# Kernel optimization log

Measured on AMD Instinct MI355X. Metric: run time of the kernel, lower is better.

## Reference

```python
import jax, jax.numpy as jnp
import numpy as np

P, A = 8, 65536            # poses, atoms per pose
N = P * A                  # total atoms
N1 = N + 1                 # kin nodes (node 0 = virtual root)


def _local_hts(dofs):
    """Per-node local homogeneous transform from bond DOFs.
    dofs[:,0]=phi (torsion), dofs[:,1]=theta (bond angle), dofs[:,2]=d (length).
    M = Rz(phi) @ Ry(theta) @ Trans_x(d)   (NeRF-style internal coordinates)."""
    phi, theta, d = dofs[:, 0], dofs[:, 1], dofs[:, 2]
    cp, sp = jnp.cos(phi), jnp.sin(phi)
    ct, st = jnp.cos(theta), jnp.sin(theta)
    z = jnp.zeros_like(phi)
    o = jnp.ones_like(phi)
    # R = Rz(phi) @ Ry(theta)
    r00, r01, r02 = cp * ct, -sp, cp * st
    r10, r11, r12 = sp * ct, cp, sp * st
    r20, r21, r22 = -st, z, ct
    # t = R @ [d,0,0]
    t0, t1, t2 = d * r00, d * r10, d * r20
    M = jnp.stack([
        jnp.stack([r00, r01, r02, t0], -1),
        jnp.stack([r10, r11, r12, t1], -1),
        jnp.stack([r20, r21, r22, t2], -1),
        jnp.stack([z, z, z, o], -1),
    ], -2)  # [N1,4,4]
    return M


def setup_inputs() -> dict:
    rng = np.random.default_rng(0)
    # tree: each node's parent is 1..4 nodes back (topologically sorted), root self-parented
    parents = np.zeros(N1, np.int32)
    idx = np.arange(1, N1)
    parents[1:] = np.maximum(idx - 1 - rng.integers(0, 4, size=N), 0).astype(np.int32)
    # kinforest.id: permutation mapping kin node (1..N) -> flat atom index
    kin_id = rng.permutation(N).astype(np.int32)
    # base DOFs (detached full_dofs): realistic bond geometry
    base = np.zeros((N1, 4), np.float32)
    base[:, 1] = rng.uniform(1.5, 2.2, N1)          # theta
    base[:, 2] = rng.normal(1.53, 0.02, N1)         # bond length
    masked = rng.uniform(-np.pi, np.pi, N1).astype(np.float32)  # torsion params
    bond_w = rng.uniform(0.5, 1.5, (P, A - 1)).astype(np.float32)
    pose_coords = np.zeros((P, A, 3), np.float32)
    return {
        "masked_dofs": jnp.asarray(masked),
        "base_dofs": jnp.asarray(base),
        "pose_coords": jnp.asarray(pose_coords),
        "bond_w": jnp.asarray(bond_w),
        "parents": jnp.asarray(parents),
        "kin_id": jnp.asarray(kin_id),
    }


def reference(masked_dofs, base_dofs, pose_coords, bond_w, parents, kin_id):
    # 1) write optimizable DOFs into full DOF tensor (dof_mask = torsion column)
    dofs = base_dofs.at[:, 0].set(masked_dofs)
    # 2) per-node local transforms; root = identity
    M = _local_hts(dofs)
    M = M.at[0].set(jnp.eye(4, dtype=M.dtype))
    # 3) forwardKin: compose parent->child transforms via pointer doubling
    n_iters = int(np.ceil(np.log2(N1)))
    def body(carry, _):
        G, p = carry
        G = jnp.einsum('nij,njk->nik', G[p], G)
        return (G, p[p]), None
    (G, _), _ = jax.lax.scan(body, (M, parents), None, length=n_iters)
    kincoords = G[1:, :3, 3]  # [N,3] global positions (skip root)
    # 4) scatter kin coords back into pose-stack coordinates
    flat = pose_coords.reshape(-1, 3).at[kin_id].set(kincoords)
    coords = flat.reshape(pose_coords.shape)  # [P,A,3]
    # 5) whole-pose scoring: weighted bonded quadratic energy per pose
    d = coords[:, 1:] - coords[:, :-1]
    energy = jnp.sum(bond_w * jnp.sum(d * d, -1), axis=-1)  # [P]
    return energy
```

## Files before the change

### kernel.cpp

```cpp
#include <hip/hip_runtime.h>

#define NN1    524289
#define PP     8
#define AA     65536
#define SEGLEN 64
#define NSEG   8193
#define CHUNK  33
#define NCHK   249
#define NE     (NCHK*4)

#define OFF_COORDS 0
#define OFF_NT   2097152
#define OFF_L1G  4194308
#define OFF_L1E  4587572
#define OFF_PREG 4620344
#define OFF_PREE 5013608
#define OFF_BCG  5046380
#define OFF_CLG  5058332
#define OFF_CLE  5070284

static __device__ __forceinline__ void set_ident(float* a){
  a[0]=1.f;a[1]=0.f;a[2]=0.f;a[3]=0.f;
  a[4]=0.f;a[5]=1.f;a[6]=0.f;a[7]=0.f;
  a[8]=0.f;a[9]=0.f;a[10]=1.f;a[11]=0.f;
}

static __device__ __forceinline__ void compose(const float* Aa, const float* B, float* O){
  #pragma unroll
  for(int r=0;r<3;r++){
    float a0=Aa[r*4+0],a1=Aa[r*4+1],a2=Aa[r*4+2],a3=Aa[r*4+3];
    O[r*4+0]=a0*B[0]+a1*B[4]+a2*B[8];
    O[r*4+1]=a0*B[1]+a1*B[5]+a2*B[9];
    O[r*4+2]=a0*B[2]+a1*B[6]+a2*B[10];
    O[r*4+3]=a0*B[3]+a1*B[7]+a2*B[11]+a3;
  }
}

static __device__ __forceinline__ void load12(const float4* b4, int idx, float* a){
  float4 x=b4[idx*3+0], y=b4[idx*3+1], z=b4[idx*3+2];
  a[0]=x.x;a[1]=x.y;a[2]=x.z;a[3]=x.w;
  a[4]=y.x;a[5]=y.y;a[6]=y.z;a[7]=y.w;
  a[8]=z.x;a[9]=z.y;a[10]=z.z;a[11]=z.w;
}
static __device__ __forceinline__ void store12(float4* b4, int idx, const float* a){
  b4[idx*3+0]=make_float4(a[0],a[1],a[2],a[3]);
  b4[idx*3+1]=make_float4(a[4],a[5],a[6],a[7]);
  b4[idx*3+2]=make_float4(a[8],a[9],a[10],a[11]);
}

static __device__ __forceinline__ void wave_scan(
    int w, int lane,
    const float* __restrict__ masked, const float4* __restrict__ base4,
    const int* __restrict__ parents,
    float G[12], int& pk)
{
  int i0 = w*SEGLEN;
  int i = i0 + lane;
  if(i == 0 || i >= NN1){
    set_ident(G); pk = 0xFF;
  } else {
    float4 b = base4[i];
    float phi = masked[i];
    float sp,cp,st,ct;
    __sincosf(phi,&sp,&cp);
    __sincosf(b.y,&st,&ct);
    float dd = b.z;
    G[0]=cp*ct; G[1]=-sp; G[2]=cp*st; G[3]=dd*G[0];
    G[4]=sp*ct; G[5]=cp;  G[6]=sp*st; G[7]=dd*G[4];
    G[8]=-st;   G[9]=0.f; G[10]=ct;   G[11]=dd*G[8];
    int rel = parents[i] - i0;
    pk = (rel >= 0) ? rel : (((rel+4)<<8) | 0xFF);
  }
  #pragma unroll
  for(int step=0; step<6; ++step){
    int ptr = pk & 0xFF;
    bool act = (ptr != 0xFF);
    int src = act ? ptr : lane;
    float g2[12];
    #pragma unroll
    for(int q=0;q<12;q++) g2[q] = __shfl(G[q], src, 64);
    int pk2 = __shfl(pk, src, 64);
    float ng[12];
    compose(g2, G, ng);
    #pragma unroll
    for(int q=0;q<12;q++) G[q] = act ? ng[q] : G[q];
    pk = act ? pk2 : pk;
  }
}

#define BSTEP(BX, EX) {                                                   \
    int s_ = s0 + q;                                                      \
    store12(PREG, s_*4+j, acc); PREE[s_*4+j] = ae;                        \
    float lg_[12];                                                        \
    _Pragma("unroll") for(int z=0;z<12;z++) lg_[z]=BX[z];                 \
    int le_ = EX;                                                         \
    if(q+3 < ns){ load12(L1G,(s_+3)*4+j, BX); EX = L1E[(s_+3)*4+j]; }     \
    int srcLane_ = laneBase + le_;                                        \
    float src_[12];                                                       \
    _Pragma("unroll") for(int z=0;z<12;z++) src_[z] = __shfl(acc[z], srcLane_, 64); \
    int se_ = __shfl(ae, srcLane_, 64);                                   \
    float nw_[12]; compose(src_, lg_, nw_);                               \
    _Pragma("unroll") for(int z=0;z<12;z++) acc[z]=nw_[z];                \
    ae = se_;                                                             \
    q++;                                                                  \
  }

static __device__ __forceinline__ void chunk_scan(
    int idx, int lane,
    const float4* __restrict__ L1G, const int* __restrict__ L1E,
    float4* __restrict__ PREG, int* __restrict__ PREE,
    float acc[12], int& ae)
{
  int g = idx>>2, j = idx&3;
  int laneBase = lane & ~3;
  int s0 = g*CHUNK;
  int ns = min(CHUNK, NSEG - s0);
  set_ident(acc); ae = j;
  float b0[12],b1[12],b2[12]; int e0=0,e1=0,e2=0;
  load12(L1G, s0*4+j, b0); e0 = L1E[s0*4+j];
  if(ns>1){ load12(L1G,(s0+1)*4+j,b1); e1 = L1E[(s0+1)*4+j]; }
  if(ns>2){ load12(L1G,(s0+2)*4+j,b2); e2 = L1E[(s0+2)*4+j]; }
  int q = 0;
  while(true){
    BSTEP(b0, e0); if(q>=ns) break;
    BSTEP(b1, e1); if(q>=ns) break;
    BSTEP(b2, e2); if(q>=ns) break;
  }
}

__global__ __launch_bounds__(1024) void fk1(
    const float* __restrict__ masked, const float4* __restrict__ base4,
    const int* __restrict__ parents,
    float4* __restrict__ L1G, int* __restrict__ L1E,
    float4* __restrict__ NT, float* __restrict__ out)
{
  if(blockIdx.x==0 && threadIdx.x < PP) out[threadIdx.x] = 0.f;
  int w = blockIdx.x*16 + (threadIdx.x>>6);
  if(w >= NSEG) return;
  int lane = threadIdx.x & 63;
  float G[12]; int pk;
  wave_scan(w, lane, masked, base4, parents, G, pk);
  int i = w*SEGLEN + lane;
  int tag = (pk>>8)&3;
  if(i < NN1){
    NT[i] = make_float4(G[3], G[7], G[11], __int_as_float(tag));
  }
  if(lane >= 60){
    int j = lane - 60;
    store12(L1G, w*4+j, G);
    L1E[w*4+j] = tag;
  }
}

__global__ __launch_bounds__(64) void fk2(
    const float4* __restrict__ L1G, const int* __restrict__ L1E,
    float4* __restrict__ PREG, int* __restrict__ PREE,
    float4* __restrict__ CLG, int* __restrict__ CLE)
{
  int idx = blockIdx.x*64 + threadIdx.x;
  if(idx >= NE) return;
  float acc[12]; int ae;
  chunk_scan(idx, threadIdx.x & 63, L1G, L1E, PREG, PREE, acc, ae);
  store12(CLG, idx, acc);
  CLE[idx] = ae;
}

__global__ __launch_bounds__(1024) void fk3(
    const float4* __restrict__ CLG, const int* __restrict__ CLE,
    float4* __restrict__ BCG)
{
  __shared__ float Lg[NE*12];
  __shared__ int   Le[NE];
  float4* Lg4 = (float4*)Lg;
  int tid = threadIdx.x;
  if(tid < NE){
    float a[12]; load12(CLG, tid, a);
    Lg4[tid*3+0]=make_float4(a[0],a[1],a[2],a[3]);
    Lg4[tid*3+1]=make_float4(a[4],a[5],a[6],a[7]);
    Lg4[tid*3+2]=make_float4(a[8],a[9],a[10],a[11]);
    Le[tid]=CLE[tid];
  }
  __syncthreads();
  for(int d=1; d<NCHK; d<<=1){
    float ng[12]; int ne2=0;
    bool doit = (tid<NE) && ((tid>>2)>=d);
    if(doit){
      int myE = Le[tid];
      int pe = ((tid>>2)-d)*4 + myE;
      float own[12], pg[12];
      load12(Lg4, tid, own);
      load12(Lg4, pe, pg);
      compose(pg, own, ng);
      ne2 = Le[pe];
    }
    __syncthreads();
    if(doit){
      Lg4[tid*3+0]=make_float4(ng[0],ng[1],ng[2],ng[3]);
      Lg4[tid*3+1]=make_float4(ng[4],ng[5],ng[6],ng[7]);
      Lg4[tid*3+2]=make_float4(ng[8],ng[9],ng[10],ng[11]);
      Le[tid]=ne2;
    }
    __syncthreads();
  }
  if(tid < NE){
    float b[12];
    if((tid>>2)==0){ set_ident(b); }
    else { load12(Lg4, tid-4, b); }
    store12(BCG, tid, b);
  }
}

__global__ __launch_bounds__(1024) void fk4(
    const int* __restrict__ kin, const float4* __restrict__ NT,
    const float4* __restrict__ PREG, const int* __restrict__ PREE,
    const float4* __restrict__ BCG,
    float4* __restrict__ coords)
{
  int w = blockIdx.x*16 + (threadIdx.x>>6);
  if(w >= NSEG) return;
  int lane = threadIdx.x & 63;
  int i = w*SEGLEN + lane;
  if(i == 0 || i >= NN1) return;
  float4 nt = NT[i];
  int tag = __float_as_int(nt.w) & 3;
  int c = w / CHUNK;
  int e = PREE[w*4+tag];
  float bg[12], pg[12], A[12];
  load12(BCG, c*4+e, bg);
  load12(PREG, w*4+tag, pg);
  compose(bg, pg, A);
  float x = A[0]*nt.x + A[1]*nt.y + A[2]*nt.z  + A[3];
  float y = A[4]*nt.x + A[5]*nt.y + A[6]*nt.z  + A[7];
  float z = A[8]*nt.x + A[9]*nt.y + A[10]*nt.z + A[11];
  coords[kin[i-1]] = make_float4(x, y, z, 0.f);
}

__global__ void fk5(const float4* __restrict__ coords, const float* __restrict__ bw,
                    float* __restrict__ out)
{
  int p = blockIdx.x >> 5;
  int sub = blockIdx.x & 31;
  int a0 = sub * 2048;
  int aend = min(a0 + 2048, AA - 1);
  float sum = 0.f;
  for(int a = a0 + (int)threadIdx.x; a < aend; a += 256){
    int r = p*AA + a;
    float4 c0 = coords[r], c1 = coords[r+1];
    float dx = c1.x-c0.x, dy = c1.y-c0.y, dz = c1.z-c0.z;
    sum += bw[p*(AA-1)+a]*(dx*dx+dy*dy+dz*dz);
  }
  #pragma unroll
  for(int off=32;off>0;off>>=1) sum += __shfl_down(sum, off, 64);
  __shared__ float red[4];
  int lane = threadIdx.x & 63, wid = threadIdx.x >> 6;
  if(lane==0) red[wid]=sum;
  __syncthreads();
  if(threadIdx.x==0){
    float tot = red[0]+red[1]+red[2]+red[3];
    atomicAdd(&out[p], tot);
  }
}

extern "C" void kernel_launch(void* const* d_in, const int* in_sizes, int n_in,
                              void* d_out, int out_size, void* d_ws, size_t ws_size,
                              hipStream_t stream)
{
  const float*  masked  = (const float*)d_in[0];
  const float4* base4   = (const float4*)d_in[1];
  const float*  bw      = (const float*)d_in[3];
  const int*    parents = (const int*)d_in[4];
  const int*    kin     = (const int*)d_in[5];

  float* ws = (float*)d_ws;
  float4* coords = (float4*)(ws + OFF_COORDS);
  float4* NT  = (float4*)(ws + OFF_NT);
  float4* L1G = (float4*)(ws + OFF_L1G);
  int*    L1E = (int*)(ws + OFF_L1E);
  float4* PREG= (float4*)(ws + OFF_PREG);
  int*    PREE= (int*)(ws + OFF_PREE);
  float4* BCG = (float4*)(ws + OFF_BCG);
  float4* CLG = (float4*)(ws + OFF_CLG);
  int*    CLE = (int*)(ws + OFF_CLE);
  float*  out = (float*)d_out;

  int nblk = (NSEG + 15) / 16;
  fk1<<<nblk, 1024, 0, stream>>>(masked, base4, parents, L1G, L1E, NT, out);
  fk2<<<(NE + 63) / 64, 64, 0, stream>>>(L1G, L1E, PREG, PREE, CLG, CLE);
  fk3<<<1, 1024, 0, stream>>>(CLG, CLE, BCG);
  fk4<<<nblk, 1024, 0, stream>>>(kin, NT, PREG, PREE, BCG, coords);
  fk5<<<PP*32, 256, 0, stream>>>(coords, bw, out);
}
```

Measured before the change: 55.44 us.

## Replace serial per-chunk segment scan with wave-parallel Hillis-Steele scan in fk2

```diff
diff --git a/kernel.cpp b/kernel.cpp
--- a/kernel.cpp
+++ b/kernel.cpp
@@ -88,46 +88,6 @@
   }
 }
 
-#define BSTEP(BX, EX) {                                                   \
-    int s_ = s0 + q;                                                      \
-    store12(PREG, s_*4+j, acc); PREE[s_*4+j] = ae;                        \
-    float lg_[12];                                                        \
-    _Pragma("unroll") for(int z=0;z<12;z++) lg_[z]=BX[z];                 \
-    int le_ = EX;                                                         \
-    if(q+3 < ns){ load12(L1G,(s_+3)*4+j, BX); EX = L1E[(s_+3)*4+j]; }     \
-    int srcLane_ = laneBase + le_;                                        \
-    float src_[12];                                                       \
-    _Pragma("unroll") for(int z=0;z<12;z++) src_[z] = __shfl(acc[z], srcLane_, 64); \
-    int se_ = __shfl(ae, srcLane_, 64);                                   \
-    float nw_[12]; compose(src_, lg_, nw_);                               \
-    _Pragma("unroll") for(int z=0;z<12;z++) acc[z]=nw_[z];                \
-    ae = se_;                                                             \
-    q++;                                                                  \
-  }
-
-static __device__ __forceinline__ void chunk_scan(
-    int idx, int lane,
-    const float4* __restrict__ L1G, const int* __restrict__ L1E,
-    float4* __restrict__ PREG, int* __restrict__ PREE,
-    float acc[12], int& ae)
-{
-  int g = idx>>2, j = idx&3;
-  int laneBase = lane & ~3;
-  int s0 = g*CHUNK;
-  int ns = min(CHUNK, NSEG - s0);
-  set_ident(acc); ae = j;
-  float b0[12],b1[12],b2[12]; int e0=0,e1=0,e2=0;
-  load12(L1G, s0*4+j, b0); e0 = L1E[s0*4+j];
-  if(ns>1){ load12(L1G,(s0+1)*4+j,b1); e1 = L1E[(s0+1)*4+j]; }
-  if(ns>2){ load12(L1G,(s0+2)*4+j,b2); e2 = L1E[(s0+2)*4+j]; }
-  int q = 0;
-  while(true){
-    BSTEP(b0, e0); if(q>=ns) break;
-    BSTEP(b1, e1); if(q>=ns) break;
-    BSTEP(b2, e2); if(q>=ns) break;
-  }
-}
-
 __global__ __launch_bounds__(1024) void fk1(
     const float* __restrict__ masked, const float4* __restrict__ base4,
     const int* __restrict__ parents,
@@ -157,12 +117,81 @@
     float4* __restrict__ PREG, int* __restrict__ PREE,
     float4* __restrict__ CLG, int* __restrict__ CLE)
 {
-  int idx = blockIdx.x*64 + threadIdx.x;
-  if(idx >= NE) return;
-  float acc[12]; int ae;
-  chunk_scan(idx, threadIdx.x & 63, L1G, L1E, PREG, PREE, acc, ae);
-  store12(CLG, idx, acc);
-  CLE[idx] = ae;
+  int g = blockIdx.x;
+  int j = threadIdx.x;
+  int s0 = g*CHUNK;
+  int ns = min(CHUNK, NSEG - s0);
+  int sj = s0 + min(j, ns-1);
+
+  float A[4][12]; int at[4];
+  #pragma unroll
+  for(int t=0;t<4;t++){
+    load12(L1G, sj*4+t, A[t]);
+    at[t] = L1E[sj*4+t];
+  }
+  if(j >= ns){
+    #pragma unroll
+    for(int t=0;t<4;t++){ set_ident(A[t]); at[t]=t; }
+  }
+
+  #pragma unroll
+  for(int step=0; step<6; ++step){
+    int d = 1<<step;
+    int src = (j >= d) ? (j - d) : j;
+    float f[4][12]; int ft[4];
+    #pragma unroll
+    for(int t=0;t<4;t++){
+      #pragma unroll
+      for(int q=0;q<12;q++) f[t][q] = __shfl(A[t][q], src, 64);
+      ft[t] = __shfl(at[t], src, 64);
+    }
+    bool act = (j >= d) && (j < ns);
+    float nA[4][12]; int nt[4];
+    #pragma unroll
+    for(int t=0;t<4;t++){
+      int tt = at[t];
+      float sel[12];
+      #pragma unroll
+      for(int q=0;q<12;q++){
+        float v01 = (tt&1) ? f[1][q] : f[0][q];
+        float v23 = (tt&1) ? f[3][q] : f[2][q];
+        sel[q] = (tt&2) ? v23 : v01;
+      }
+      compose(sel, A[t], nA[t]);
+      int t01 = (tt&1) ? ft[1] : ft[0];
+      int t23 = (tt&1) ? ft[3] : ft[2];
+      nt[t] = (tt&2) ? t23 : t01;
+    }
+    #pragma unroll
+    for(int t=0;t<4;t++){
+      #pragma unroll
+      for(int q=0;q<12;q++) A[t][q] = act ? nA[t][q] : A[t][q];
+      at[t] = act ? nt[t] : at[t];
+    }
+  }
+
+  if(j == 0){
+    float I[12]; set_ident(I);
+    #pragma unroll
+    for(int t=0;t<4;t++){
+      store12(PREG, s0*4+t, I);
+      PREE[s0*4+t] = t;
+    }
+  }
+  if(j < ns-1){
+    #pragma unroll
+    for(int t=0;t<4;t++){
+      store12(PREG, (s0+j+1)*4+t, A[t]);
+      PREE[(s0+j+1)*4+t] = at[t];
+    }
+  }
+  if(j == ns-1){
+    #pragma unroll
+    for(int t=0;t<4;t++){
+      store12(CLG, g*4+t, A[t]);
+      CLE[g*4+t] = at[t];
+    }
+  }
 }
 
 __global__ __launch_bounds__(1024) void fk3(
@@ -285,7 +314,7 @@
 
   int nblk = (NSEG + 15) / 16;
   fk1<<<nblk, 1024, 0, stream>>>(masked, base4, parents, L1G, L1E, NT, out);
-  fk2<<<(NE + 63) / 64, 64, 0, stream>>>(L1G, L1E, PREG, PREE, CLG, CLE);
+  fk2<<<NCHK, 64, 0, stream>>>(L1G, L1E, PREG, PREE, CLG, CLE);
   fk3<<<1, 1024, 0, stream>>>(CLG, CLE, BCG);
   fk4<<<nblk, 1024, 0, stream>>>(kin, NT, PREG, PREE, BCG, coords);
   fk5<<<PP*32, 256, 0, stream>>>(coords, bw, out);
```

Measured after the change: 50.38 us. 1.1x faster.
